# Optimization experiments

Measured on AMD Instinct MI355X. Metric: run time of the kernel, lower is better.

Reference implementation:

```python
import jax, jax.numpy as jnp
import numpy as np

N = 100_000          # nodes
DEG = 16             # avg degree (random edges)
E = N * DEG + N      # edges incl. self-loops (ensures no zero in-degree)
NFEAT = 256
NHID = 64
NHEADS = 8
NCLASS = 40
NEG_SLOPE = 0.2
S_F = 1.0
EPS = 1e-6


def setup_inputs() -> dict:
    key = jax.random.key(0)
    ks = jax.random.split(key, 12)
    x = jax.random.normal(ks[0], (N, NFEAT), dtype=jnp.float32)
    loops = jnp.arange(N, dtype=jnp.int32)
    src = jnp.concatenate([jax.random.randint(ks[1], (N * DEG,), 0, N, dtype=jnp.int32), loops])
    dst = jnp.concatenate([jax.random.randint(ks[2], (N * DEG,), 0, N, dtype=jnp.int32), loops])
    # layer-1: NHEADS independent single-head GATConv_G(nfeat -> nhid)
    W1 = (jax.random.normal(ks[3], (NHEADS, NHID, NFEAT), dtype=jnp.float32) * 0.05)
    al1 = jax.random.normal(ks[4], (NHEADS, NHID), dtype=jnp.float32) * 0.05
    ar1 = jax.random.normal(ks[5], (NHEADS, NHID), dtype=jnp.float32) * 0.05
    b1 = jnp.zeros((NHEADS, NHID), dtype=jnp.float32)
    p1 = jax.random.normal(ks[6], (NHEADS,), dtype=jnp.float32) * 0.1
    # layer-2: single-head GATConv_G(nhid*nheads -> nclass)
    W2 = jax.random.normal(ks[7], (NCLASS, NHID * NHEADS), dtype=jnp.float32) * 0.05
    al2 = jax.random.normal(ks[8], (NCLASS,), dtype=jnp.float32) * 0.05
    ar2 = jax.random.normal(ks[9], (NCLASS,), dtype=jnp.float32) * 0.05
    b2 = jnp.zeros((NCLASS,), dtype=jnp.float32)
    p2 = jax.random.normal(ks[10], (), dtype=jnp.float32) * 0.1
    return dict(x=x, src=src, dst=dst, W1=W1, al1=al1, ar1=ar1, b1=b1, p1=p1,
                W2=W2, al2=al2, ar2=ar2, b2=b2, p2=p2)


def _leaky_relu(x):
    return jnp.where(x >= 0, x, NEG_SLOPE * x)


def _edge_softmax(e, dst):
    # softmax over incoming edges of each destination node
    m = jax.ops.segment_max(e, dst, num_segments=N)
    ex = jnp.exp(e - m[dst])
    s = jax.ops.segment_sum(ex, dst, num_segments=N)
    return ex / s[dst]


def _gat_g_head(x, src, dst, W, al, ar, b, p):
    """One GATConv_G with num_heads=1. x:[N,Fin], W:[Fout,Fin] -> [N,Fout]."""
    ft = x @ W.T                                   # [N,Fout]
    el = ft @ al                                   # [N]
    er = ft @ ar                                   # [N]
    e = _leaky_relu(el[src] + er[dst])             # [E]
    a = _edge_softmax(e, dst)                      # [E]
    pe = jax.nn.sigmoid(p) + S_F                   # scalar, nonlinear-aggregation exponent
    mu = ft.min()                                  # global min (shift to make base positive)
    pf = jnp.power(ft - mu + EPS, pe)              # [N,Fout]
    msg = pf[src] * a[:, None]                     # [E,Fout] (u_mul_e)
    agg = jax.ops.segment_sum(msg, dst, num_segments=N)   # sum aggregation
    rst = jnp.power(agg + EPS, 1.0 / pe) + mu      # generalized-mean inverse
    return rst + b                                 # bias [Fout]


def reference(x, src, dst, W1, al1, ar1, b1, p1, W2, al2, ar2, b2, p2):
    # layer 1: NHEADS single-head GATConv_G, each with concat=True => elu, then concat
    heads = []
    for h in range(NHEADS):  # small fixed loop over structurally distinct heads
        heads.append(jax.nn.elu(_gat_g_head(x, src, dst, W1[h], al1[h], ar1[h], b1[h], p1[h])))
    hcat = jnp.concatenate(heads, axis=-1)         # [N, NHEADS*NHID]
    # layer 2: output GATConv_G (concat=False), then log_softmax classifier head
    out = _gat_g_head(hcat, src, dst, W2, al2, ar2, b2, p2)   # [N, NCLASS]
    return jax.nn.log_softmax(out, axis=-1)
```

## Files before the change

kernel.cpp:

```cpp
#include <hip/hip_runtime.h>

#define NN 100000
#define EE 1700000
#define F1 256
#define NH 8
#define HF 64
#define C1 512
#define C2 40
#define EPS 1e-6f

#define OF_PF1   ((size_t)0)
#define OF_HCAT  (OF_PF1  + 102400000ULL)
#define OF_FT2   (OF_HCAT + 102400000ULL)
#define OF_EL1   (OF_FT2  + 16000000ULL)
#define OF_ER1   (OF_EL1  + 3200000ULL)
#define OF_EL2   (OF_ER1  + 3200000ULL)
#define OF_ER2   (OF_EL2  + 400000ULL)
#define OF_DEG   (OF_ER2  + 400000ULL)
#define OF_OFFS  (OF_DEG  + 400000ULL)
#define OF_CUR   (OF_OFFS + 400128ULL)
#define OF_SRCC  (OF_CUR  + 400000ULL)
#define OF_BSUM  (OF_SRCC + 6800000ULL)
#define OF_BOFF  (OF_BSUM + 2048ULL)
#define OF_PRM   (OF_BOFF + 2048ULL)
#define OF_W2H   (OF_PRM  + 1024ULL)
#define OF_XH    (OF_HCAT)
#define OF_WH    (OF_HCAT + 51200000ULL)


typedef _Float16 f16x8 __attribute__((ext_vector_type(8)));
typedef _Float16 f16x4 __attribute__((ext_vector_type(4)));
typedef float f32x4 __attribute__((ext_vector_type(4)));

__device__ __forceinline__ unsigned f2key(float f){
  unsigned u = __float_as_uint(f);
  return (u & 0x80000000u) ? ~u : (u | 0x80000000u);
}
__device__ __forceinline__ float key2f(unsigned k){
  unsigned u = (k & 0x80000000u) ? (k & 0x7FFFFFFFu) : ~k;
  return __uint_as_float(u);
}
__device__ __forceinline__ unsigned short f2b(float f){
  unsigned u = __float_as_uint(f);
  unsigned r = u + 0x7FFFu + ((u >> 16) & 1u);
  return (unsigned short)(r >> 16);
}
__device__ __forceinline__ float b2f(unsigned short b){
  return __uint_as_float(((unsigned)b) << 16);
}
__device__ __forceinline__ float leaky(float e){ return e >= 0.f ? e : 0.2f*e; }

__device__ __forceinline__ void gload16(const _Float16* g, char* l){
  __builtin_amdgcn_global_load_lds((const __attribute__((address_space(1))) void*)g,
                                   (__attribute__((address_space(3))) void*)l, 16, 0, 0);
}

__global__ void k_init(const float* __restrict__ p1, const float* __restrict__ p2, unsigned* __restrict__ prm){
  int t = threadIdx.x;
  float* prf = (float*)prm;
  if (t < 8){
    prm[t] = 0xFFFFFFFFu;
    float pe = 1.f/(1.f + __expf(-p1[t])) + 1.0f;
    prf[16 + t] = pe;
    prf[24 + t] = 1.f/pe;
  }
  if (t == 0){
    prm[8] = 0xFFFFFFFFu;
    float pe = 1.f/(1.f + __expf(-p2[0])) + 1.0f;
    prf[32] = pe;
    prf[33] = 1.f/pe;
  }
}

__global__ void k_zero_deg(int* __restrict__ deg){
  int i = blockIdx.x*256 + threadIdx.x;
  if (i < NN) deg[i] = 0;
}

__global__ void k_cvt16(const float* __restrict__ in, _Float16* __restrict__ out){
  int i = blockIdx.x*256 + threadIdx.x;
  const float4* p = (const float4*)in + (size_t)i*2;
  float4 a = p[0], b = p[1];
  f16x8 h = {(_Float16)a.x,(_Float16)a.y,(_Float16)a.z,(_Float16)a.w,
             (_Float16)b.x,(_Float16)b.y,(_Float16)b.z,(_Float16)b.w};
  *((f16x8*)out + i) = h;
}

__global__ void k_cvtW2(const float* __restrict__ W2, _Float16* __restrict__ W2h){
  int i = blockIdx.x*256 + threadIdx.x;
  int row = i >> 9, col = i & 511;
  W2h[i] = (row < C2) ? (_Float16)W2[row*C1 + col] : (_Float16)0.f;
}

#define G1_BM 128
#define G1_BN 128
#define G1_BK 64
__global__ __launch_bounds__(256) void k_gemm1(const _Float16* __restrict__ xh, const _Float16* __restrict__ Wh,
                                               unsigned short* __restrict__ ft1b, unsigned* __restrict__ prm){
  __shared__ __align__(16) char smem[35840];
  char* Abase = smem;
  char* Bbase = smem + 16384;
  unsigned short (*Cs)[136] = (unsigned short (*)[136])smem;

  int t = threadIdx.x;
  int lane = t & 63, w = t >> 6;
  int wr = w >> 1, wc = w & 1;
  int ct = blockIdx.x * G1_BN;
  int rt = blockIdx.y * G1_BM;

  int lr8 = lane >> 3;
  int gcs = (lane & 7) ^ lr8;

  f32x4 zero = {0.f,0.f,0.f,0.f};
  f32x4 acc[4][4];
  #pragma unroll
  for (int m=0;m<4;m++)
    #pragma unroll
    for (int n=0;n<4;n++) acc[m][n] = zero;

  for (int kt = 0; kt < F1; kt += G1_BK){
    #pragma unroll
    for (int i = 0; i < 4; i++){
      int ch = w*4 + i;
      int row = ch*8 + lr8;
      int ga = min(rt + row, NN-1);
      gload16(xh + (size_t)ga*F1 + kt + gcs*8, Abase + ch*1024);
      gload16(Wh + (size_t)(ct+row)*F1 + kt + gcs*8, Bbase + ch*1024);
    }
    __syncthreads();
    #pragma unroll
    for (int kk = 0; kk < 2; kk++){
      f16x8 af[4], bf[4];
      #pragma unroll
      for (int m=0;m<4;m++){
        int row = wr*64 + m*16 + (lane & 15);
        int g = kk*4 + (lane >> 4);
        af[m] = *(f16x8*)(Abase + ((row*8 + (g ^ (row & 7)))<<4));
      }
      #pragma unroll
      for (int n=0;n<4;n++){
        int row = wc*64 + n*16 + (lane & 15);
        int g = kk*4 + (lane >> 4);
        bf[n] = *(f16x8*)(Bbase + ((row*8 + (g ^ (row & 7)))<<4));
      }
      #pragma unroll
      for (int m=0;m<4;m++)
        #pragma unroll
        for (int n=0;n<4;n++)
          acc[m][n] = __builtin_amdgcn_mfma_f32_16x16x32_f16(af[m], bf[n], acc[m][n], 0, 0, 0);
    }
    __syncthreads();
  }

  int h = (ct >> 6) + wc;
  unsigned kmin = 0xFFFFFFFFu;
  #pragma unroll
  for (int m=0;m<4;m++){
    #pragma unroll
    for (int n=0;n<4;n++){
      int cl = wc*64 + n*16 + (lane & 15);
      int rl = wr*64 + m*16 + (lane >> 4)*4;
      #pragma unroll
      for (int j=0;j<4;j++){
        unsigned short ub = f2b(acc[m][n][j]);
        Cs[rl + j][cl] = ub;
        kmin = min(kmin, f2key(b2f(ub)));
      }
    }
  }
  #pragma unroll
  for (int off=1; off<64; off<<=1) kmin = min(kmin, (unsigned)__shfl_xor((int)kmin, off));
  if (lane == 0) atomicMin(&prm[h], kmin);
  __syncthreads();

  #pragma unroll
  for (int p = 0; p < 8; p++){
    int flat = p*256 + t;
    int row = flat >> 4;
    int q   = flat & 15;
    int gr = rt + row;
    if (gr < NN){
      uint4 v = *(const uint4*)&Cs[row][q*8];
      *(uint4*)&ft1b[(size_t)gr*C1 + ct + q*8] = v;
    }
  }
}

__global__ void k_count(const int* __restrict__ dst, int* __restrict__ deg){
  int e = blockIdx.x*256 + threadIdx.x;
  if (e < EE) atomicAdd(&deg[dst[e]], 1);
}
__global__ void k_scan1(const int* __restrict__ deg, int* __restrict__ offs, int* __restrict__ bsum){
  __shared__ int s[256];
  int t = threadIdx.x; int i = blockIdx.x*256 + t;
  int v = (i < NN) ? deg[i] : 0;
  s[t] = v; __syncthreads();
  for (int off=1; off<256; off<<=1){
    int tmp = (t>=off) ? s[t-off] : 0;
    __syncthreads(); s[t] += tmp; __syncthreads();
  }
  if (i < NN) offs[i] = s[t] - v;
  if (t == 255) bsum[blockIdx.x] = s[255];
}
__global__ void k_scan2(int* __restrict__ bsum, int* __restrict__ boff, int nb){
  __shared__ int s[512];
  int t = threadIdx.x;
  int v = (t < nb) ? bsum[t] : 0;
  s[t] = v; __syncthreads();
  for (int off=1; off<512; off<<=1){
    int tmp = (t>=off) ? s[t-off] : 0;
    __syncthreads(); s[t] += tmp; __syncthreads();
  }
  if (t < nb) boff[t] = s[t] - v;
}
__global__ void k_scan3(int* __restrict__ offs, int* __restrict__ cur, const int* __restrict__ boff){
  int i = blockIdx.x*256 + threadIdx.x;
  if (i < NN){
    int v = offs[i] + boff[blockIdx.x];
    offs[i] = v; cur[i] = v;
  }
  if (i == 0) offs[NN] = EE;
}
__global__ void k_fill(const int* __restrict__ src, const int* __restrict__ dst,
                       int* __restrict__ cur, int* __restrict__ srcc){
  int e = blockIdx.x*256 + threadIdx.x;
  if (e < EE){
    int d = dst[e];
    int pos = atomicAdd(&cur[d], 1);
    srcc[pos] = src[e];
  }
}

__global__ __launch_bounds__(256) void k_transform1(unsigned short* __restrict__ ft1b,
    const float* __restrict__ al1, const float* __restrict__ ar1,
    float* __restrict__ el1, float* __restrict__ er1, const unsigned* __restrict__ prm){
  int lane = threadIdx.x & 63; int w = threadIdx.x >> 6;
  int n = blockIdx.x*4 + w;
  if (n >= NN) return;
  const float* prf = (const float*)prm;
  float vv[8], elp[8], erp[8];
  #pragma unroll
  for (int h=0; h<8; h++){
    vv[h]  = b2f(ft1b[(size_t)n*C1 + h*HF + lane]);
    elp[h] = vv[h]*al1[h*HF + lane];
    erp[h] = vv[h]*ar1[h*HF + lane];
  }
  #pragma unroll
  for (int h=0; h<8; h++){
    #pragma unroll
    for (int off=1; off<64; off<<=1){
      elp[h] += __shfl_xor(elp[h], off);
      erp[h] += __shfl_xor(erp[h], off);
    }
  }
  if (lane == 0){
    #pragma unroll
    for (int h=0; h<8; h++){ el1[(size_t)n*8+h]=elp[h]; er1[(size_t)n*8+h]=erp[h]; }
  }
  #pragma unroll
  for (int h=0; h<8; h++){
    float mu = key2f(prm[h]);
    float pe = prf[16+h];
    float base = vv[h] - mu + EPS;
    ft1b[(size_t)n*C1 + h*HF + lane] = f2b(__expf(pe * __logf(base)));
  }
}

__global__ __launch_bounds__(256) void k_agg1(const unsigned short* __restrict__ pf1b,
    const float* __restrict__ el1, const float* __restrict__ er1,
    const int* __restrict__ offs, const int* __restrict__ srcc,
    const float* __restrict__ b1, const unsigned* __restrict__ prm,
    _Float16* __restrict__ hcath){
  int lane = threadIdx.x & 63; int w = threadIdx.x >> 6;
  int v = blockIdx.x*4 + w;
  if (v >= NN) return;
  const float* prf = (const float*)prm;
  int h = lane >> 3;
  int s = lane & 7;
  int start = offs[v], end = offs[v+1];
  float erh = er1[(size_t)v*8 + h];

  float m = -INFINITY;
  for (int pos = start + s; pos < end; pos += 8){
    int u = srcc[pos];
    float e = leaky(el1[(size_t)u*8 + h] + erh);
    m = fmaxf(m, e);
  }
  m = fmaxf(m, __shfl_xor(m,1)); m = fmaxf(m, __shfl_xor(m,2)); m = fmaxf(m, __shfl_xor(m,4));
  float S = 0.f;
  for (int pos = start + s; pos < end; pos += 8){
    int u = srcc[pos];
    float e = leaky(el1[(size_t)u*8 + h] + erh);
    S += __expf(e - m);
  }
  S += __shfl_xor(S,1); S += __shfl_xor(S,2); S += __shfl_xor(S,4);
  float invS = 1.f / S;

  int es = lane >> 5;
  int hc = (lane >> 2) & 7;
  int q4 = lane & 3;
  float mh    = __shfl(m,    hc*8);
  float invSh = __shfl(invS, hc*8);
  float erhc  = __shfl(erh,  hc*8);

  float acc[16];
  #pragma unroll
  for (int j=0;j<16;j++) acc[j]=0.f;
  for (int pos = start + es; pos < end; pos += 2){
    int u = srcc[pos];
    float e = leaky(el1[(size_t)u*8 + hc] + erhc);
    float a = __expf(e - mh) * invSh;
    const unsigned short* pr = &pf1b[(size_t)u*C1 + hc*HF + q4*16];
    uint4 qa = *(const uint4*)pr;
    uint4 qb = *(const uint4*)(pr + 8);
    acc[0]  += a*b2f((unsigned short)(qa.x & 0xFFFFu));
    acc[1]  += a*b2f((unsigned short)(qa.x >> 16));
    acc[2]  += a*b2f((unsigned short)(qa.y & 0xFFFFu));
    acc[3]  += a*b2f((unsigned short)(qa.y >> 16));
    acc[4]  += a*b2f((unsigned short)(qa.z & 0xFFFFu));
    acc[5]  += a*b2f((unsigned short)(qa.z >> 16));
    acc[6]  += a*b2f((unsigned short)(qa.w & 0xFFFFu));
    acc[7]  += a*b2f((unsigned short)(qa.w >> 16));
    acc[8]  += a*b2f((unsigned short)(qb.x & 0xFFFFu));
    acc[9]  += a*b2f((unsigned short)(qb.x >> 16));
    acc[10] += a*b2f((unsigned short)(qb.y & 0xFFFFu));
    acc[11] += a*b2f((unsigned short)(qb.y >> 16));
    acc[12] += a*b2f((unsigned short)(qb.z & 0xFFFFu));
    acc[13] += a*b2f((unsigned short)(qb.z >> 16));
    acc[14] += a*b2f((unsigned short)(qb.w & 0xFFFFu));
    acc[15] += a*b2f((unsigned short)(qb.w >> 16));
  }
  #pragma unroll
  for (int j=0;j<16;j++) acc[j] += __shfl_xor(acc[j], 32);

  float mu = key2f(prm[hc]);
  float ipe = prf[24+hc];
  int fb = q4*16 + es*8;
  f16x8 o;
  #pragma unroll
  for (int j=0;j<8;j++){
    float r = __expf(ipe * __logf(acc[es*8 + j] + EPS)) + mu + b1[hc*HF + fb + j];
    o[j] = (_Float16)((r > 0.f) ? r : (__expf(r) - 1.f));
  }
  *(f16x8*)&hcath[(size_t)v*C1 + hc*HF + fb] = o;
}

__global__ __launch_bounds__(256) void k_gemm2(const _Float16* __restrict__ hcath, const _Float16* __restrict__ W2h,
    float* __restrict__ ft2, float* __restrict__ el2, float* __restrict__ er2,
    const float* __restrict__ al2, const float* __restrict__ ar2, unsigned* __restrict__ prm){
  __shared__ __align__(16) char smem[45056];
  char* Abase = smem;
  char* Bbase = smem + 32768;
  __shared__ unsigned mk;
  int t = threadIdx.x;
  int lane = t & 63, w = t >> 6;
  int rt = blockIdx.x * 128;
  if (t == 0) mk = 0xFFFFFFFFu;

  f32x4 zero = {0.f,0.f,0.f,0.f};
  f32x4 acc[2][3];
  #pragma unroll
  for (int m=0;m<2;m++)
    #pragma unroll
    for (int n=0;n<3;n++) acc[m][n] = zero;

  for (int step = 0; step < 4; step++){
    #pragma unroll
    for (int p = 0; p < 8; p++){
      int idx = p*256 + t;
      int row = idx >> 4, g = idx & 15;
      int ga = min(rt + row, NN-1);
      gload16(hcath + (size_t)ga*C1 + step*128 + ((g ^ (row & 7))<<3), Abase + idx*16);
    }
    #pragma unroll
    for (int p = 0; p < 3; p++){
      int idx = p*256 + t;
      int row = idx >> 4, g = idx & 15;
      gload16(W2h + (size_t)row*C1 + step*128 + ((g ^ (row & 7))<<3), Bbase + idx*16);
    }
    __syncthreads();
    #pragma unroll
    for (int kk = 0; kk < 4; kk++){
      f16x8 af[2], bf[3];
      #pragma unroll
      for (int m=0;m<2;m++){
        int row = w*32 + m*16 + (lane & 15);
        int g = kk*4 + (lane >> 4);
        af[m] = *(f16x8*)(Abase + ((row*16 + (g ^ (row & 7)))<<4));
      }
      #pragma unroll
      for (int n=0;n<3;n++){
        int row = n*16 + (lane & 15);
        int g = kk*4 + (lane >> 4);
        bf[n] = *(f16x8*)(Bbase + ((row*16 + (g ^ (row & 7)))<<4));
      }
      #pragma unroll
      for (int m=0;m<2;m++)
        #pragma unroll
        for (int n=0;n<3;n++)
          acc[m][n] = __builtin_amdgcn_mfma_f32_16x16x32_f16(af[m], bf[n], acc[m][n], 0, 0, 0);
    }
    __syncthreads();
  }

  int c0 = lane & 15;
  unsigned kmin = 0xFFFFFFFFu;
  #pragma unroll
  for (int m=0;m<2;m++){
    float elp[4] = {0.f,0.f,0.f,0.f};
    float erp[4] = {0.f,0.f,0.f,0.f};
    #pragma unroll
    for (int n=0;n<3;n++){
      int col = n*16 + c0;
      bool okc = (col < C2);
      float alc = okc ? al2[col] : 0.f;
      float arc = okc ? ar2[col] : 0.f;
      int rbase = rt + w*32 + m*16 + (lane >> 4)*4;
      #pragma unroll
      for (int j=0;j<4;j++){
        float vv = acc[m][n][j];
        int row = rbase + j;
        if (okc && row < NN){
          ft2[(size_t)row*C2 + col] = vv;
          elp[j] += vv*alc; erp[j] += vv*arc;
          kmin = min(kmin, f2key(vv));
        }
      }
    }
    #pragma unroll
    for (int j=0;j<4;j++){
      #pragma unroll
      for (int off=1; off<16; off<<=1){
        elp[j] += __shfl_xor(elp[j], off);
        erp[j] += __shfl_xor(erp[j], off);
      }
      int row = rt + w*32 + m*16 + (lane >> 4)*4 + j;
      if (c0 == 0 && row < NN){ el2[row] = elp[j]; er2[row] = erp[j]; }
    }
  }
  #pragma unroll
  for (int off=1; off<64; off<<=1) kmin = min(kmin, (unsigned)__shfl_xor((int)kmin, off));
  if (lane == 0) atomicMin(&mk, kmin);
  __syncthreads();
  if (t == 0) atomicMin(&prm[8], mk);
}

__global__ void k_transform2(float* __restrict__ ft2, const unsigned* __restrict__ prm){
  int i = blockIdx.x*256 + threadIdx.x;
  if (i >= NN*C2) return;
  const float* prf = (const float*)prm;
  float mu = key2f(prm[8]);
  float pe = prf[32];
  float v = ft2[i];
  ft2[i] = __expf(pe * __logf(v - mu + EPS));
}

__global__ __launch_bounds__(256) void k_agg2(const float* __restrict__ pf2,
    const float* __restrict__ el2, const float* __restrict__ er2,
    const int* __restrict__ offs, const int* __restrict__ srcc,
    const float* __restrict__ b2, const unsigned* __restrict__ prm,
    float* __restrict__ out){
  int lane = threadIdx.x & 63; int w = threadIdx.x >> 6;
  int v = blockIdx.x*4 + w;
  if (v >= NN) return;
  const float* prf = (const float*)prm;
  int start = offs[v], end = offs[v+1];
  float erv = er2[v];

  float m = -INFINITY;
  for (int pos = start + lane; pos < end; pos += 64){
    float e = leaky(el2[srcc[pos]] + erv);
    m = fmaxf(m, e);
  }
  #pragma unroll
  for (int off=1; off<64; off<<=1) m = fmaxf(m, __shfl_xor(m, off));
  float S = 0.f;
  for (int pos = start + lane; pos < end; pos += 64){
    float e = leaky(el2[srcc[pos]] + erv);
    S += __expf(e - m);
  }
  #pragma unroll
  for (int off=1; off<64; off<<=1) S += __shfl_xor(S, off);
  float invS = 1.f / S;

  int s = lane >> 4;
  int c = lane & 15;
  float a0=0.f, a1=0.f, a2=0.f, a3=0.f;
  for (int pos = start + s; pos < end; pos += 4){
    int u = srcc[pos];
    float a = __expf(leaky(el2[u] + erv) - m) * invS;
    if (c < 10){
      float4 q = *(const float4*)&pf2[(size_t)u*C2 + c*4];
      a0 += a*q.x; a1 += a*q.y; a2 += a*q.z; a3 += a*q.w;
    }
  }
  a0 += __shfl_xor(a0,16); a1 += __shfl_xor(a1,16); a2 += __shfl_xor(a2,16); a3 += __shfl_xor(a3,16);
  a0 += __shfl_xor(a0,32); a1 += __shfl_xor(a1,32); a2 += __shfl_xor(a2,32); a3 += __shfl_xor(a3,32);

  float y[4];
  float mx;
  if (c < 10){
    float mu = key2f(prm[8]);
    float ipe = prf[33];
    float av[4] = {a0,a1,a2,a3};
    #pragma unroll
    for (int j=0;j<4;j++) y[j] = __expf(ipe * __logf(av[j] + EPS)) + mu + b2[c*4 + j];
    mx = fmaxf(fmaxf(y[0],y[1]), fmaxf(y[2],y[3]));
  } else {
    y[0]=y[1]=y[2]=y[3]=-INFINITY;
    mx = -INFINITY;
  }
  mx = fmaxf(mx, __shfl_xor(mx,1)); mx = fmaxf(mx, __shfl_xor(mx,2));
  mx = fmaxf(mx, __shfl_xor(mx,4)); mx = fmaxf(mx, __shfl_xor(mx,8));
  float se = 0.f;
  if (c < 10){
    #pragma unroll
    for (int j=0;j<4;j++) se += __expf(y[j] - mx);
  }
  se += __shfl_xor(se,1); se += __shfl_xor(se,2); se += __shfl_xor(se,4); se += __shfl_xor(se,8);
  float ls = __logf(se);
  if (s == 0 && c < 10){
    float4 o = make_float4(y[0]-mx-ls, y[1]-mx-ls, y[2]-mx-ls, y[3]-mx-ls);
    *(float4*)&out[(size_t)v*C2 + c*4] = o;
  }
}

extern "C" void kernel_launch(void* const* d_in, const int* in_sizes, int n_in,
                              void* d_out, int out_size, void* d_ws, size_t ws_size,
                              hipStream_t stream){
  const float* x   = (const float*)d_in[0];
  const int*   src = (const int*)d_in[1];
  const int*   dst = (const int*)d_in[2];
  const float* W1  = (const float*)d_in[3];
  const float* al1 = (const float*)d_in[4];
  const float* ar1 = (const float*)d_in[5];
  const float* b1  = (const float*)d_in[6];
  const float* p1  = (const float*)d_in[7];
  const float* W2  = (const float*)d_in[8];
  const float* al2 = (const float*)d_in[9];
  const float* ar2 = (const float*)d_in[10];
  const float* b2  = (const float*)d_in[11];
  const float* p2  = (const float*)d_in[12];
  float* out = (float*)d_out;
  char* ws = (char*)d_ws;

  unsigned short* pf1b  = (unsigned short*)(ws + OF_PF1);
  _Float16* hcath = (_Float16*)(ws + OF_HCAT);
  _Float16* xh  = (_Float16*)(ws + OF_XH);
  _Float16* Wh  = (_Float16*)(ws + OF_WH);
  _Float16* W2h = (_Float16*)(ws + OF_W2H);
  float* ft2   = (float*)(ws + OF_FT2);
  float* el1   = (float*)(ws + OF_EL1);
  float* er1   = (float*)(ws + OF_ER1);
  float* el2   = (float*)(ws + OF_EL2);
  float* er2   = (float*)(ws + OF_ER2);
  int*   deg   = (int*)(ws + OF_DEG);
  int*   offs  = (int*)(ws + OF_OFFS);
  int*   cur   = (int*)(ws + OF_CUR);
  int*   srcc  = (int*)(ws + OF_SRCC);
  int*   bsum  = (int*)(ws + OF_BSUM);
  int*   boff  = (int*)(ws + OF_BOFF);
  unsigned* prm = (unsigned*)(ws + OF_PRM);

  const int NB1 = (NN + 255)/256;
  const int NBE = (EE + 255)/256;

  k_init<<<1, 64, 0, stream>>>(p1, p2, prm);
  k_zero_deg<<<NB1, 256, 0, stream>>>(deg);
  k_cvt16<<<12500, 256, 0, stream>>>(x, xh);
  k_cvt16<<<64, 256, 0, stream>>>(W1, Wh);
  k_cvtW2<<<96, 256, 0, stream>>>(W2, W2h);
  k_gemm1<<<dim3(C1/G1_BN, (NN + G1_BM - 1)/G1_BM), 256, 0, stream>>>(xh, Wh, pf1b, prm);
  k_count<<<NBE, 256, 0, stream>>>(dst, deg);
  k_scan1<<<NB1, 256, 0, stream>>>(deg, offs, bsum);
  k_scan2<<<1, 512, 0, stream>>>(bsum, boff, NB1);
  k_scan3<<<NB1, 256, 0, stream>>>(offs, cur, boff);
  k_fill<<<NBE, 256, 0, stream>>>(src, dst, cur, srcc);
  k_transform1<<<NN/4, 256, 0, stream>>>(pf1b, al1, ar1, el1, er1, prm);
  k_agg1<<<NN/4, 256, 0, stream>>>(pf1b, el1, er1, offs, srcc, b1, prm, hcath);
  k_gemm2<<<(NN + 127)/128, 256, 0, stream>>>(hcath, W2h, ft2, el2, er2, al2, ar2, prm);
  k_transform2<<<(NN*C2 + 255)/256, 256, 0, stream>>>(ft2, prm);
  k_agg2<<<NN/4, 256, 0, stream>>>(ft2, el2, er2, offs, srcc, b2, prm, out);
}
```

Before: 896.8 us.

## Fuse attention logits into GEMM1 epilogue, vectorize pf1 power, store pf2 as fp16

```diff
diff --git a/kernel.cpp b/kernel.cpp
--- a/kernel.cpp
+++ b/kernel.cpp
@@ -26,6 +26,7 @@
 #define OF_W2H   (OF_PRM  + 1024ULL)
 #define OF_XH    (OF_HCAT)
 #define OF_WH    (OF_HCAT + 51200000ULL)
+#define OF_PF2H  (OF_HCAT)
 
 
 typedef _Float16 f16x8 __attribute__((ext_vector_type(8)));
@@ -96,7 +97,10 @@
 #define G1_BN 128
 #define G1_BK 64
 __global__ __launch_bounds__(256) void k_gemm1(const _Float16* __restrict__ xh, const _Float16* __restrict__ Wh,
-                                               unsigned short* __restrict__ ft1b, unsigned* __restrict__ prm){
+                                               const float* __restrict__ al1, const float* __restrict__ ar1,
+                                               unsigned short* __restrict__ ft1b,
+                                               float* __restrict__ el1, float* __restrict__ er1,
+                                               unsigned* __restrict__ prm){
   __shared__ __align__(16) char smem[35840];
   char* Abase = smem;
   char* Bbase = smem + 16384;
@@ -153,18 +157,43 @@
   }
 
   int h = (ct >> 6) + wc;
+  int c0 = lane & 15;
+  float alc[4], arc[4];
+  #pragma unroll
+  for (int n=0;n<4;n++){
+    alc[n] = al1[h*HF + n*16 + c0];
+    arc[n] = ar1[h*HF + n*16 + c0];
+  }
   unsigned kmin = 0xFFFFFFFFu;
   #pragma unroll
   for (int m=0;m<4;m++){
+    float elp[4] = {0.f,0.f,0.f,0.f};
+    float erp[4] = {0.f,0.f,0.f,0.f};
     #pragma unroll
     for (int n=0;n<4;n++){
-      int cl = wc*64 + n*16 + (lane & 15);
+      int cl = wc*64 + n*16 + c0;
       int rl = wr*64 + m*16 + (lane >> 4)*4;
       #pragma unroll
       for (int j=0;j<4;j++){
         unsigned short ub = f2b(acc[m][n][j]);
+        float vr = b2f(ub);
         Cs[rl + j][cl] = ub;
-        kmin = min(kmin, f2key(b2f(ub)));
+        kmin = min(kmin, f2key(vr));
+        elp[j] += vr*alc[n];
+        erp[j] += vr*arc[n];
+      }
+    }
+    #pragma unroll
+    for (int j=0;j<4;j++){
+      #pragma unroll
+      for (int off=1; off<16; off<<=1){
+        elp[j] += __shfl_xor(elp[j], off);
+        erp[j] += __shfl_xor(erp[j], off);
+      }
+      int row = rt + wr*64 + m*16 + (lane >> 4)*4 + j;
+      if (c0 == 0 && row < NN){
+        el1[(size_t)row*8 + h] = elp[j];
+        er1[(size_t)row*8 + h] = erp[j];
       }
     }
   }
@@ -231,39 +260,28 @@
   }
 }
 
-__global__ __launch_bounds__(256) void k_transform1(unsigned short* __restrict__ ft1b,
-    const float* __restrict__ al1, const float* __restrict__ ar1,
-    float* __restrict__ el1, float* __restrict__ er1, const unsigned* __restrict__ prm){
-  int lane = threadIdx.x & 63; int w = threadIdx.x >> 6;
-  int n = blockIdx.x*4 + w;
-  if (n >= NN) return;
+__global__ void k_pf1(unsigned short* __restrict__ ft1b, const unsigned* __restrict__ prm){
+  int i = blockIdx.x*256 + threadIdx.x;
   const float* prf = (const float*)prm;
-  float vv[8], elp[8], erp[8];
-  #pragma unroll
-  for (int h=0; h<8; h++){
-    vv[h]  = b2f(ft1b[(size_t)n*C1 + h*HF + lane]);
-    elp[h] = vv[h]*al1[h*HF + lane];
-    erp[h] = vv[h]*ar1[h*HF + lane];
-  }
-  #pragma unroll
-  for (int h=0; h<8; h++){
-    #pragma unroll
-    for (int off=1; off<64; off<<=1){
-      elp[h] += __shfl_xor(elp[h], off);
-      erp[h] += __shfl_xor(erp[h], off);
-    }
-  }
-  if (lane == 0){
-    #pragma unroll
-    for (int h=0; h<8; h++){ el1[(size_t)n*8+h]=elp[h]; er1[(size_t)n*8+h]=erp[h]; }
-  }
-  #pragma unroll
-  for (int h=0; h<8; h++){
-    float mu = key2f(prm[h]);
-    float pe = prf[16+h];
-    float base = vv[h] - mu + EPS;
-    ft1b[(size_t)n*C1 + h*HF + lane] = f2b(__expf(pe * __logf(base)));
-  }
+  int h = (i >> 3) & 7;
+  float mu = key2f(prm[h]);
+  float pe = prf[16 + h];
+  uint4 q = ((const uint4*)ft1b)[i];
+  unsigned r0, r1, r2, r3;
+  float v0, v1;
+  v0 = b2f((unsigned short)(q.x & 0xFFFFu)) - mu + EPS;
+  v1 = b2f((unsigned short)(q.x >> 16)) - mu + EPS;
+  r0 = (unsigned)f2b(__expf(pe*__logf(v0))) | ((unsigned)f2b(__expf(pe*__logf(v1))) << 16);
+  v0 = b2f((unsigned short)(q.y & 0xFFFFu)) - mu + EPS;
+  v1 = b2f((unsigned short)(q.y >> 16)) - mu + EPS;
+  r1 = (unsigned)f2b(__expf(pe*__logf(v0))) | ((unsigned)f2b(__expf(pe*__logf(v1))) << 16);
+  v0 = b2f((unsigned short)(q.z & 0xFFFFu)) - mu + EPS;
+  v1 = b2f((unsigned short)(q.z >> 16)) - mu + EPS;
+  r2 = (unsigned)f2b(__expf(pe*__logf(v0))) | ((unsigned)f2b(__expf(pe*__logf(v1))) << 16);
+  v0 = b2f((unsigned short)(q.w & 0xFFFFu)) - mu + EPS;
+  v1 = b2f((unsigned short)(q.w >> 16)) - mu + EPS;
+  r3 = (unsigned)f2b(__expf(pe*__logf(v0))) | ((unsigned)f2b(__expf(pe*__logf(v1))) << 16);
+  ((uint4*)ft1b)[i] = make_uint4(r0, r1, r2, r3);
 }
 
 __global__ __launch_bounds__(256) void k_agg1(const unsigned short* __restrict__ pf1b,
@@ -445,17 +463,18 @@
   if (t == 0) atomicMin(&prm[8], mk);
 }
 
-__global__ void k_transform2(float* __restrict__ ft2, const unsigned* __restrict__ prm){
+__global__ void k_transform2(const float* __restrict__ ft2, _Float16* __restrict__ pf2h,
+                             const unsigned* __restrict__ prm){
   int i = blockIdx.x*256 + threadIdx.x;
   if (i >= NN*C2) return;
   const float* prf = (const float*)prm;
   float mu = key2f(prm[8]);
   float pe = prf[32];
   float v = ft2[i];
-  ft2[i] = __expf(pe * __logf(v - mu + EPS));
-}
-
-__global__ __launch_bounds__(256) void k_agg2(const float* __restrict__ pf2,
+  pf2h[i] = (_Float16)__expf(pe * __logf(v - mu + EPS));
+}
+
+__global__ __launch_bounds__(256) void k_agg2(const _Float16* __restrict__ pf2h,
     const float* __restrict__ el2, const float* __restrict__ er2,
     const int* __restrict__ offs, const int* __restrict__ srcc,
     const float* __restrict__ b2, const unsigned* __restrict__ prm,
@@ -490,8 +509,8 @@
     int u = srcc[pos];
     float a = __expf(leaky(el2[u] + erv) - m) * invS;
     if (c < 10){
-      float4 q = *(const float4*)&pf2[(size_t)u*C2 + c*4];
-      a0 += a*q.x; a1 += a*q.y; a2 += a*q.z; a3 += a*q.w;
+      f16x4 q = *(const f16x4*)&pf2h[(size_t)u*C2 + c*4];
+      a0 += a*(float)q[0]; a1 += a*(float)q[1]; a2 += a*(float)q[2]; a3 += a*(float)q[3];
     }
   }
   a0 += __shfl_xor(a0,16); a1 += __shfl_xor(a1,16); a2 += __shfl_xor(a2,16); a3 += __shfl_xor(a3,16);
@@ -549,6 +568,7 @@
   _Float16* xh  = (_Float16*)(ws + OF_XH);
   _Float16* Wh  = (_Float16*)(ws + OF_WH);
   _Float16* W2h = (_Float16*)(ws + OF_W2H);
+  _Float16* pf2h = (_Float16*)(ws + OF_PF2H);
   float* ft2   = (float*)(ws + OF_FT2);
   float* el1   = (float*)(ws + OF_EL1);
   float* er1   = (float*)(ws + OF_ER1);
@@ -570,15 +590,15 @@
   k_cvt16<<<12500, 256, 0, stream>>>(x, xh);
   k_cvt16<<<64, 256, 0, stream>>>(W1, Wh);
   k_cvtW2<<<96, 256, 0, stream>>>(W2, W2h);
-  k_gemm1<<<dim3(C1/G1_BN, (NN + G1_BM - 1)/G1_BM), 256, 0, stream>>>(xh, Wh, pf1b, prm);
+  k_gemm1<<<dim3(C1/G1_BN, (NN + G1_BM - 1)/G1_BM), 256, 0, stream>>>(xh, Wh, al1, ar1, pf1b, el1, er1, prm);
   k_count<<<NBE, 256, 0, stream>>>(dst, deg);
   k_scan1<<<NB1, 256, 0, stream>>>(deg, offs, bsum);
   k_scan2<<<1, 512, 0, stream>>>(bsum, boff, NB1);
   k_scan3<<<NB1, 256, 0, stream>>>(offs, cur, boff);
   k_fill<<<NBE, 256, 0, stream>>>(src, dst, cur, srcc);
-  k_transform1<<<NN/4, 256, 0, stream>>>(pf1b, al1, ar1, el1, er1, prm);
+  k_pf1<<<25000, 256, 0, stream>>>(pf1b, prm);
   k_agg1<<<NN/4, 256, 0, stream>>>(pf1b, el1, er1, offs, srcc, b1, prm, hcath);
   k_gemm2<<<(NN + 127)/128, 256, 0, stream>>>(hcath, W2h, ft2, el2, er2, al2, ar2, prm);
-  k_transform2<<<(NN*C2 + 255)/256, 256, 0, stream>>>(ft2, prm);
-  k_agg2<<<NN/4, 256, 0, stream>>>(ft2, el2, er2, offs, srcc, b2, prm, out);
-}
+  k_transform2<<<(NN*C2 + 255)/256, 256, 0, stream>>>(ft2, pf2h, prm);
+  k_agg2<<<NN/4, 256, 0, stream>>>(pf2h, el2, er2, offs, srcc, b2, prm, out);
+}
```

Measured after the change: 861.7 us. -3.9%, faster.
